# Kernel optimization log

Hardware: AMD Instinct MI355X
Metric: run time of the kernel (lower is better)

Reference implementation:

```python
import jax, jax.numpy as jnp
import numpy as np

STRIDES = (8, 16, 32)
BINS = 16
NC = 80
ALPHA, GAMMA = 0.25, 2.0
W_CLS, W_IOU, W_DFL = 1.0, 7.5, 1.5
B, MAX_GT = 32, 32
EPS = 1e-7


def setup_inputs() -> dict:
    key = jax.random.key(0)
    k0, k1, k2, k3, k4, k5, k6 = jax.random.split(key, 7)
    p0 = jax.random.normal(k0, (B, 4 * BINS + NC, 80, 80), dtype=jnp.float32)
    p1 = jax.random.normal(k1, (B, 4 * BINS + NC, 40, 40), dtype=jnp.float32)
    p2 = jax.random.normal(k2, (B, 4 * BINS + NC, 20, 20), dtype=jnp.float32)
    # realistic xyxy boxes inside a 640x640 image
    c = jax.random.uniform(k3, (B, MAX_GT, 2), minval=60.0, maxval=580.0)
    wh = jax.random.uniform(k4, (B, MAX_GT, 2), minval=16.0, maxval=120.0)
    gt_bboxes = jnp.concatenate([c - wh / 2, c + wh / 2], axis=-1).astype(jnp.float32)
    gt_labels = jax.random.randint(k5, (B, MAX_GT), 0, NC, dtype=jnp.int32)
    raw = jax.random.randint(k6, (B, 8400), 0, 20 * MAX_GT, dtype=jnp.int32)
    matched_gt_inds = jnp.where(raw < MAX_GT, raw, -1)
    return {"p0": p0, "p1": p1, "p2": p2, "gt_bboxes": gt_bboxes,
            "gt_labels": gt_labels, "matched_gt_inds": matched_gt_inds}


def _decode_scale(p, stride):
    # p: [B, 4*BINS + NC, H, W]
    Bp, C, H, W = p.shape
    dfl = p[:, :4 * BINS].reshape(Bp, 4, BINS, H, W)
    cls = p[:, 4 * BINS:]
    # DFL decode: expectation of softmax over bins, scaled by stride
    prob = jax.nn.softmax(dfl, axis=2)
    proj = jnp.arange(BINS, dtype=p.dtype)
    dist = jnp.einsum('bkchw,c->bkhw', prob, proj) * stride  # [B,4,H,W] in pixels
    ys, xs = jnp.meshgrid(jnp.arange(H), jnp.arange(W), indexing='ij')
    cx = ((xs.astype(p.dtype)) + 0.5) * stride
    cy = ((ys.astype(p.dtype)) + 0.5) * stride
    boxes = jnp.stack([cx - dist[:, 0], cy - dist[:, 1],
                       cx + dist[:, 2], cy + dist[:, 3]], axis=-1).reshape(Bp, H * W, 4)
    cls_logits = cls.transpose(0, 2, 3, 1).reshape(Bp, H * W, NC)
    dfl_flat = dfl.transpose(0, 3, 4, 1, 2).reshape(Bp, H * W, 4, BINS)
    grid = jnp.stack([cx, cy], axis=-1).reshape(H * W, 2)
    smap = jnp.full((H * W,), stride, dtype=p.dtype)
    return cls_logits, dfl_flat, boxes, grid, smap


def reference(p0, p1, p2, gt_bboxes, gt_labels, matched_gt_inds):
    outs = [_decode_scale(p, s) for p, s in zip((p0, p1, p2), STRIDES)]
    scores = jnp.concatenate([o[0] for o in outs], axis=1)   # [B,N,NC]
    dfl = jnp.concatenate([o[1] for o in outs], axis=1)      # [B,N,4,BINS]
    pboxes = jnp.concatenate([o[2] for o in outs], axis=1)   # [B,N,4]
    grid = jnp.concatenate([o[3] for o in outs], axis=0)     # [N,2]
    smap = jnp.concatenate([o[4] for o in outs], axis=0)     # [N]

    pos = matched_gt_inds >= 0                               # [B,N]
    idx = jnp.where(pos, matched_gt_inds, 0)
    lbl = jnp.take_along_axis(gt_labels, idx, axis=1)        # [B,N]
    posf = pos.astype(scores.dtype)
    tgt_scores = jax.nn.one_hot(lbl, NC, dtype=scores.dtype) * posf[..., None]

    # sigmoid focal loss (stable BCE-with-logits)
    prob = jax.nn.sigmoid(scores)
    ce = jnp.maximum(scores, 0) - scores * tgt_scores + jnp.log1p(jnp.exp(-jnp.abs(scores)))
    p_t = prob * tgt_scores + (1 - prob) * (1 - tgt_scores)
    alpha_t = tgt_scores * ALPHA + (1 - tgt_scores) * (1 - ALPHA)
    cls_elem = alpha_t * (1.0 - p_t) ** GAMMA * ce
    num_pos = jnp.maximum(posf.sum(), 1.0)
    loss_cls = cls_elem.sum() / num_pos

    # gather matched GT boxes per anchor
    tboxes = jnp.take_along_axis(gt_bboxes, idx[..., None], axis=1)  # [B,N,4]
    gx, gy = grid[None, :, 0], grid[None, :, 1]
    l = jnp.clip(gx - tboxes[..., 0], 0.0)
    t = jnp.clip(gy - tboxes[..., 1], 0.0)
    r = jnp.clip(tboxes[..., 2] - gx, 0.0)
    b_ = jnp.clip(tboxes[..., 3] - gy, 0.0)
    dists = jnp.stack([l, t, r, b_], axis=-1) / smap[None, :, None]   # [B,N,4]
    tb = jnp.clip(dists, 0.0, BINS - 1 - 1e-6)
    lo = jnp.floor(tb).astype(jnp.int32)
    hi = jnp.minimum(lo + 1, BINS - 1)
    a = tb - lo.astype(tb.dtype)
    # soft two-bin DFL target (vectorized form of the scatter_add loop)
    tdist = (jax.nn.one_hot(lo, BINS, dtype=dfl.dtype) * (1.0 - a)[..., None]
             + jax.nn.one_hot(hi, BINS, dtype=dfl.dtype) * a[..., None])   # [B,N,4,BINS]
    logp = jax.nn.log_softmax(dfl, axis=-1)
    dfl_elem = -(tdist * logp).sum(-1)                                # [B,N,4]
    loss_dfl = (dfl_elem * posf[..., None]).sum() / (num_pos * 4.0)

    # IoU loss on positives
    ix1 = jnp.maximum(pboxes[..., 0], tboxes[..., 0])
    iy1 = jnp.maximum(pboxes[..., 1], tboxes[..., 1])
    ix2 = jnp.minimum(pboxes[..., 2], tboxes[..., 2])
    iy2 = jnp.minimum(pboxes[..., 3], tboxes[..., 3])
    inter = jnp.clip(ix2 - ix1, 0.0) * jnp.clip(iy2 - iy1, 0.0)
    area_p = jnp.clip(pboxes[..., 2] - pboxes[..., 0], 0.0) * jnp.clip(pboxes[..., 3] - pboxes[..., 1], 0.0)
    area_t = jnp.clip(tboxes[..., 2] - tboxes[..., 0], 0.0) * jnp.clip(tboxes[..., 3] - tboxes[..., 1], 0.0)
    iou = inter / (area_p + area_t - inter + EPS)
    loss_iou = ((1.0 - iou) * posf).sum() / num_pos

    total = W_CLS * loss_cls + W_IOU * loss_iou + W_DFL * loss_dfl
    return total
```

## Files before the change

### kernel.cpp

```cpp
#include <hip/hip_runtime.h>
#include <math.h>

#define NCLS 80
#define BINS 16
#define BATCH 32
#define MAX_GT 32
#define NA 8400
#define AN (BATCH * NA)
#define NT 2100
#define NB_DFL 1050
#define NB_CLS 2560
#define NSLOT 64
#define ALPHA_C 0.25f
#define W_CLS 1.0
#define W_IOU 7.5
#define W_DFL 1.5
#define EPS_F 1e-7f


__device__ __forceinline__ void block_reduce_atomic(float val, double* __restrict__ target)
{
    __shared__ float s[4];
    __syncthreads();
    #pragma unroll
    for (int o = 32; o > 0; o >>= 1) val += __shfl_down(val, o);
    const int wave = threadIdx.x >> 6, lane = threadIdx.x & 63;
    if (lane == 0) s[wave] = val;
    __syncthreads();
    if (threadIdx.x == 0) atomicAdd(target, (double)(s[0] + s[1] + s[2] + s[3]));
}

__device__ __forceinline__ float focal_elem(float s, float tt)
{
    float e   = __expf(-fabsf(s));
    float inv = 1.f / (1.f + e);
    float prob = (s >= 0.f) ? inv : e * inv;
    float ce  = fmaxf(s, 0.f) - s * tt + __logf(1.f + e);
    float p_t = prob * tt + (1.f - prob) * (1.f - tt);
    float alpha_t = tt * ALPHA_C + (1.f - tt) * (1.f - ALPHA_C);
    float om = 1.f - p_t;
    return alpha_t * om * om * ce;
}

__global__ __launch_bounds__(256) void yolo_prep(
    const int* __restrict__ matched, const int* __restrict__ gt_labels,
    signed char* __restrict__ lblmap, double* __restrict__ acc)
{
    if (blockIdx.x == 0) acc[threadIdx.x] = 0.0;
    const int qid = blockIdx.x * 256 + threadIdx.x;
    if (qid >= AN / 4) return;
    const int a0 = qid * 4;
    const int b  = a0 / NA;
    const int4 m4 = *(const int4*)(matched + a0);
    const int mm[4] = {m4.x, m4.y, m4.z, m4.w};
    char4 o;
    o.x = (mm[0] >= 0) ? (signed char)gt_labels[b * MAX_GT + mm[0]] : (signed char)-1;
    o.y = (mm[1] >= 0) ? (signed char)gt_labels[b * MAX_GT + mm[1]] : (signed char)-1;
    o.z = (mm[2] >= 0) ? (signed char)gt_labels[b * MAX_GT + mm[2]] : (signed char)-1;
    o.w = (mm[3] >= 0) ? (signed char)gt_labels[b * MAX_GT + mm[3]] : (signed char)-1;
    *(char4*)(lblmap + a0) = o;
}

__global__ __launch_bounds__(256) void yolo_mega(
    const float* __restrict__ p0, const float* __restrict__ p1, const float* __restrict__ p2,
    const float* __restrict__ gt_bboxes, const int* __restrict__ matched,
    const signed char* __restrict__ lblmap, double* __restrict__ acc)
{
    const int bid  = blockIdx.x;
    const int slot = bid & (NSLOT - 1);

    if (bid < NB_DFL) {
        __shared__ float spd[64][4][4];
        const int gdt = bid * 256 + (int)threadIdx.x;
        const int k   = gdt & 3;
        const int qg  = gdt >> 2;
        const int b   = qg / NT;
        const int t   = qg - b * NT;

        const float* p; int HW, off, gbase, h, w0; float stride;
        if (t < 1600)      { p = p0; HW = 6400; off = t * 4;          gbase = 0;    stride = 8.f;
                             h = t / 20;  w0 = (t - h * 20) * 4; }
        else if (t < 2000) { p = p1; HW = 1600; off = (t - 1600) * 4; gbase = 6400; stride = 16.f;
                             int u = t - 1600; h = u / 10; w0 = (u - h * 10) * 4; }
        else               { p = p2; HW = 400;  off = (t - 2000) * 4; gbase = 8000; stride = 32.f;
                             int u = t - 2000; h = u / 5;  w0 = (u - h * 5) * 4; }
        const float inv_s = 1.f / stride;
        const float cy = ((float)h + 0.5f) * stride;

        const float* pc = p + (size_t)(b * 144 + k * BINS) * HW + off;
        float v[BINS][4];
        #pragma unroll
        for (int i = 0; i < BINS; ++i) {
            float4 q = *(const float4*)(pc + (size_t)i * HW);
            v[i][0] = q.x; v[i][1] = q.y; v[i][2] = q.z; v[i][3] = q.w;
        }
        const int4 m4 = *(const int4*)(matched + (size_t)b * NA + gbase + off);
        const int mm[4] = {m4.x, m4.y, m4.z, m4.w};
        bool pos[4]; float4 tbv[4]; float tdv[4];
        #pragma unroll
        for (int j = 0; j < 4; ++j) {
            pos[j] = (mm[j] >= 0);
            int idx = pos[j] ? mm[j] : 0;
            tbv[j] = *(const float4*)(gt_bboxes + ((size_t)b * MAX_GT + idx) * 4);
            float cx = ((float)(w0 + j) + 0.5f) * stride;
            float d = (k == 0) ? (cx - tbv[j].x) : (k == 1) ? (cy - tbv[j].y)
                    : (k == 2) ? (tbv[j].z - cx) : (tbv[j].w - cy);
            tdv[j] = fmaxf(d, 0.f) * inv_s;
        }

        float part = 0.f;
        float pd[4];
        #pragma unroll
        for (int j = 0; j < 4; ++j) {
            float tval = fminf(tdv[j], (float)(BINS - 1) - 1e-6f);
            int   lo = (int)floorf(tval);
            float fr = tval - (float)lo;
            float mx = v[0][j];
            #pragma unroll
            for (int i = 1; i < BINS; ++i) mx = fmaxf(mx, v[i][j]);
            float se = 0.f, we = 0.f, vlo = 0.f, vhi = 0.f;
            #pragma unroll
            for (int i = 0; i < BINS; ++i) {
                float e = __expf(v[i][j] - mx);
                se += e;
                we += (float)i * e;
                vlo = (i == lo)     ? v[i][j] : vlo;
                vhi = (i == lo + 1) ? v[i][j] : vhi;
            }
            pd[j] = (we / se) * stride;
            if (pos[j]) {
                float lse = mx + __logf(se);
                part += -((1.f - fr) * (vlo - lse) + fr * (vhi - lse));
            }
        }
        *(float4*)&spd[threadIdx.x >> 2][k][0] = make_float4(pd[0], pd[1], pd[2], pd[3]);
        __syncthreads();

        float iou_part = 0.f, cnt = 0.f;
        if (k == 0) {
            const int g = threadIdx.x >> 2;
            #pragma unroll
            for (int j = 0; j < 4; ++j) {
                if (pos[j]) {
                    float cx = ((float)(w0 + j) + 0.5f) * stride;
                    float px1 = cx - spd[g][0][j], py1 = cy - spd[g][1][j];
                    float px2 = cx + spd[g][2][j], py2 = cy + spd[g][3][j];
                    float4 tb = tbv[j];
                    float ix1 = fmaxf(px1, tb.x), iy1 = fmaxf(py1, tb.y);
                    float ix2 = fminf(px2, tb.z), iy2 = fminf(py2, tb.w);
                    float inter  = fmaxf(ix2 - ix1, 0.f) * fmaxf(iy2 - iy1, 0.f);
                    float area_p = fmaxf(px2 - px1, 0.f) * fmaxf(py2 - py1, 0.f);
                    float area_t = fmaxf(tb.z - tb.x, 0.f) * fmaxf(tb.w - tb.y, 0.f);
                    float iou = inter / (area_p + area_t - inter + EPS_F);
                    iou_part += 1.f - iou;
                    cnt += 1.f;
                }
            }
        }
        block_reduce_atomic(part,     &acc[2 * NSLOT + slot]);
        block_reduce_atomic(iou_part, &acc[1 * NSLOT + slot]);
        block_reduce_atomic(cnt,      &acc[3 * NSLOT + slot]);
    } else {
        const int cbid = bid - NB_DFL;
        const int b = cbid / NCLS;
        const int c = cbid - b * NCLS;
        const size_t cls_ch = (size_t)(b * 144 + 4 * BINS + c);
        const signed char* lb0 = lblmap + b * NA;

        float4 q[9];
        char4  l4[9];
        const float* pl0 = p0 + cls_ch * 6400;
        #pragma unroll
        for (int i = 0; i < 6; ++i) {
            int off = (i * 256 + (int)threadIdx.x) * 4;
            q[i]  = *(const float4*)(pl0 + off);
            l4[i] = *(const char4*)(lb0 + off);
        }
        #pragma unroll
        for (int i = 6; i < 9; ++i) {
            int t  = i * 256 + (int)threadIdx.x;
            int tc = (t < NT) ? t : 0;
            const float* p; int HW, off, gbase;
            if (tc < 1600)      { p = p0; HW = 6400; off = tc * 4;          gbase = 0;    }
            else if (tc < 2000) { p = p1; HW = 1600; off = (tc - 1600) * 4; gbase = 6400; }
            else                { p = p2; HW = 400;  off = (tc - 2000) * 4; gbase = 8000; }
            q[i]  = *(const float4*)(p + cls_ch * HW + off);
            l4[i] = *(const char4*)(lb0 + gbase + off);
        }

        float part = 0.f;
        #pragma unroll
        for (int i = 0; i < 9; ++i) {
            const bool valid = (i < 8) || (i * 256 + (int)threadIdx.x < NT);
            const float s4[4]  = {q[i].x, q[i].y, q[i].z, q[i].w};
            const int   lbl[4] = {l4[i].x, l4[i].y, l4[i].z, l4[i].w};
            float sum = 0.f;
            #pragma unroll
            for (int j = 0; j < 4; ++j)
                sum += focal_elem(s4[j], (c == lbl[j]) ? 1.f : 0.f);
            part += valid ? sum : 0.f;
        }
        block_reduce_atomic(part, &acc[0 * NSLOT + slot]);
    }
}

__global__ __launch_bounds__(256) void yolo_loss_fused(
    const float* __restrict__ p0, const float* __restrict__ p1, const float* __restrict__ p2,
    const float* __restrict__ gt_bboxes, const int* __restrict__ gt_labels,
    const int* __restrict__ matched, double* __restrict__ acc)
{
    const int a = blockIdx.x * blockDim.x + threadIdx.x;
    const int b = blockIdx.y;
    const int slot = blockIdx.x & (NSLOT - 1);
    float cls_acc = 0.f, iou_acc = 0.f, dfl_acc = 0.f, pos_cnt = 0.f;
    if (a < NA) {
        const float* p; int HW, W; float stride; int off;
        if (a < 6400)      { p = p0; HW = 6400; W = 80; stride = 8.f;  off = a; }
        else if (a < 8000) { p = p1; HW = 1600; W = 40; stride = 16.f; off = a - 6400; }
        else               { p = p2; HW = 400;  W = 20; stride = 32.f; off = a - 8000; }
        const int h = off / W, w = off - h * W;
        const float cx = ((float)w + 0.5f) * stride, cy = ((float)h + 0.5f) * stride;
        const float* pb = p + ((size_t)b * 144) * (size_t)HW + (size_t)off;
        const int m = matched[(size_t)b * NA + a];
        const bool pos = (m >= 0);
        const int idx = pos ? m : 0;
        const int lbl = gt_labels[b * MAX_GT + idx];
        const float* tbp = gt_bboxes + ((size_t)b * MAX_GT + idx) * 4;
        const float tx1 = tbp[0], ty1 = tbp[1], tx2 = tbp[2], ty2 = tbp[3];
        float tdist[4] = {fmaxf(cx - tx1, 0.f) / stride, fmaxf(cy - ty1, 0.f) / stride,
                          fmaxf(tx2 - cx, 0.f) / stride, fmaxf(ty2 - cy, 0.f) / stride};
        float pdv[4]; float dfl_sum = 0.f;
        #pragma unroll
        for (int k = 0; k < 4; ++k) {
            float tv = fminf(tdist[k], (float)(BINS - 1) - 1e-6f);
            int lo = (int)floorf(tv);
            float fr = tv - (float)lo;
            const float* pc = pb + (size_t)(k * BINS) * HW;
            float v[BINS];
            #pragma unroll
            for (int i = 0; i < BINS; ++i) v[i] = pc[(size_t)i * HW];
            float mx = v[0];
            #pragma unroll
            for (int i = 1; i < BINS; ++i) mx = fmaxf(mx, v[i]);
            float se = 0.f, we = 0.f, vlo = 0.f, vhi = 0.f;
            #pragma unroll
            for (int i = 0; i < BINS; ++i) {
                float e = __expf(v[i] - mx);
                se += e; we += (float)i * e;
                vlo = (i == lo) ? v[i] : vlo;
                vhi = (i == lo + 1) ? v[i] : vhi;
            }
            pdv[k] = (we / se) * stride;
            if (pos) { float lse = mx + __logf(se); dfl_sum += -((1.f - fr) * (vlo - lse) + fr * (vhi - lse)); }
        }
        const float* pcls = pb + (size_t)(4 * BINS) * HW;
        #pragma unroll 4
        for (int c = 0; c < NCLS; ++c)
            cls_acc += focal_elem(pcls[(size_t)c * HW], (pos && c == lbl) ? 1.f : 0.f);
        if (pos) {
            float px1 = cx - pdv[0], py1 = cy - pdv[1], px2 = cx + pdv[2], py2 = cy + pdv[3];
            float ix1 = fmaxf(px1, tx1), iy1 = fmaxf(py1, ty1);
            float ix2 = fminf(px2, tx2), iy2 = fminf(py2, ty2);
            float inter  = fmaxf(ix2 - ix1, 0.f) * fmaxf(iy2 - iy1, 0.f);
            float area_p = fmaxf(px2 - px1, 0.f) * fmaxf(py2 - py1, 0.f);
            float area_t = fmaxf(tx2 - tx1, 0.f) * fmaxf(ty2 - ty1, 0.f);
            float iou = inter / (area_p + area_t - inter + EPS_F);
            iou_acc = 1.f - iou; dfl_acc = dfl_sum; pos_cnt = 1.f;
        }
    }
    block_reduce_atomic(cls_acc, &acc[0 * NSLOT + slot]);
    block_reduce_atomic(iou_acc, &acc[1 * NSLOT + slot]);
    block_reduce_atomic(dfl_acc, &acc[2 * NSLOT + slot]);
    block_reduce_atomic(pos_cnt, &acc[3 * NSLOT + slot]);
}

__global__ void yolo_loss_finalize(const double* __restrict__ acc, float* __restrict__ out)
{
    double s[4] = {0.0, 0.0, 0.0, 0.0};
    for (int q = 0; q < 4; ++q)
        for (int i = 0; i < NSLOT; ++i) s[q] += acc[q * NSLOT + i];
    double np = s[3] < 1.0 ? 1.0 : s[3];
    double total = W_CLS * s[0] / np + W_IOU * s[1] / np + W_DFL * s[2] / (np * 4.0);
    out[0] = (float)total;
}

extern "C" void kernel_launch(void* const* d_in, const int* in_sizes, int n_in,
                              void* d_out, int out_size, void* d_ws, size_t ws_size,
                              hipStream_t stream)
{
    const float* p0        = (const float*)d_in[0];
    const float* p1        = (const float*)d_in[1];
    const float* p2        = (const float*)d_in[2];
    const float* gt_bboxes = (const float*)d_in[3];
    const int*   gt_labels = (const int*)d_in[4];
    const int*   matched   = (const int*)d_in[5];
    float*  out = (float*)d_out;

    const size_t accBytes = 4 * NSLOT * sizeof(double);
    double*      acc    = (double*)d_ws;
    signed char* lblmap = (signed char*)((char*)d_ws + accBytes);
    const size_t need = accBytes + (size_t)AN;

    if (ws_size >= need) {
        yolo_prep<<<(AN / 4 + 255) / 256, 256, 0, stream>>>(matched, gt_labels, lblmap, acc);
        yolo_mega<<<NB_DFL + NB_CLS, 256, 0, stream>>>(p0, p1, p2, gt_bboxes, matched,
                                                       lblmap, acc);
    } else {
        (void)hipMemsetAsync(acc, 0, accBytes, stream);
        dim3 g((NA + 255) / 256, BATCH);
        yolo_loss_fused<<<g, 256, 0, stream>>>(p0, p1, p2, gt_bboxes, gt_labels, matched, acc);
    }
    yolo_loss_finalize<<<1, 1, 0, stream>>>(acc, out);
}
```

Before: 215.6 us.

## Drop label-map prep via focal correction, online softmax, per-block partials

Removes the label-map prep kernel. The class branch now computes the focal loss assuming every target is zero, and the DFL branch adds a per-positive correction term (focal(t=1) - focal(t=0)) at the matched label's logit. The DFL softmax becomes a streaming online max/sum over groups of four bins, and the two target-bin logits are reloaded instead of kept in registers. Shared-memory exchange of distances is replaced by wave shuffles, and the atomic slot accumulation is replaced by per-block partial writes reduced in a parallel finalize kernel. The intent is to cut a launch, byte-map traffic, register pressure and atomics, in exchange for a few extra scattered loads.

```diff
diff --git a/kernel.cpp b/kernel.cpp
--- a/kernel.cpp
+++ b/kernel.cpp
@@ -10,25 +10,13 @@
 #define NT 2100
 #define NB_DFL 1050
 #define NB_CLS 2560
+#define NBLK (NB_DFL + NB_CLS)
 #define NSLOT 64
 #define ALPHA_C 0.25f
 #define W_CLS 1.0
 #define W_IOU 7.5
 #define W_DFL 1.5
 #define EPS_F 1e-7f
-
-
-__device__ __forceinline__ void block_reduce_atomic(float val, double* __restrict__ target)
-{
-    __shared__ float s[4];
-    __syncthreads();
-    #pragma unroll
-    for (int o = 32; o > 0; o >>= 1) val += __shfl_down(val, o);
-    const int wave = threadIdx.x >> 6, lane = threadIdx.x & 63;
-    if (lane == 0) s[wave] = val;
-    __syncthreads();
-    if (threadIdx.x == 0) atomicAdd(target, (double)(s[0] + s[1] + s[2] + s[3]));
-}
 
 __device__ __forceinline__ float focal_elem(float s, float tt)
 {
@@ -42,35 +30,37 @@
     return alpha_t * om * om * ce;
 }
 
-__global__ __launch_bounds__(256) void yolo_prep(
-    const int* __restrict__ matched, const int* __restrict__ gt_labels,
-    signed char* __restrict__ lblmap, double* __restrict__ acc)
-{
-    if (blockIdx.x == 0) acc[threadIdx.x] = 0.0;
-    const int qid = blockIdx.x * 256 + threadIdx.x;
-    if (qid >= AN / 4) return;
-    const int a0 = qid * 4;
-    const int b  = a0 / NA;
-    const int4 m4 = *(const int4*)(matched + a0);
-    const int mm[4] = {m4.x, m4.y, m4.z, m4.w};
-    char4 o;
-    o.x = (mm[0] >= 0) ? (signed char)gt_labels[b * MAX_GT + mm[0]] : (signed char)-1;
-    o.y = (mm[1] >= 0) ? (signed char)gt_labels[b * MAX_GT + mm[1]] : (signed char)-1;
-    o.z = (mm[2] >= 0) ? (signed char)gt_labels[b * MAX_GT + mm[2]] : (signed char)-1;
-    o.w = (mm[3] >= 0) ? (signed char)gt_labels[b * MAX_GT + mm[3]] : (signed char)-1;
-    *(char4*)(lblmap + a0) = o;
+__device__ __forceinline__ void block_write4(float c0, float c1, float c2, float c3,
+                                             double* __restrict__ blk)
+{
+    #pragma unroll
+    for (int o = 32; o > 0; o >>= 1) {
+        c0 += __shfl_down(c0, o);
+        c1 += __shfl_down(c1, o);
+        c2 += __shfl_down(c2, o);
+        c3 += __shfl_down(c3, o);
+    }
+    __shared__ float s4[4][4];
+    const int wave = threadIdx.x >> 6, lane = threadIdx.x & 63;
+    if (lane == 0) { s4[wave][0] = c0; s4[wave][1] = c1; s4[wave][2] = c2; s4[wave][3] = c3; }
+    __syncthreads();
+    if (threadIdx.x == 0) {
+        double* o = blk + (size_t)blockIdx.x * 4;
+        o[0] = (double)(s4[0][0] + s4[1][0] + s4[2][0] + s4[3][0]);
+        o[1] = (double)(s4[0][1] + s4[1][1] + s4[2][1] + s4[3][1]);
+        o[2] = (double)(s4[0][2] + s4[1][2] + s4[2][2] + s4[3][2]);
+        o[3] = (double)(s4[0][3] + s4[1][3] + s4[2][3] + s4[3][3]);
+    }
 }
 
 __global__ __launch_bounds__(256) void yolo_mega(
     const float* __restrict__ p0, const float* __restrict__ p1, const float* __restrict__ p2,
-    const float* __restrict__ gt_bboxes, const int* __restrict__ matched,
-    const signed char* __restrict__ lblmap, double* __restrict__ acc)
-{
-    const int bid  = blockIdx.x;
-    const int slot = bid & (NSLOT - 1);
+    const float* __restrict__ gt_bboxes, const int* __restrict__ gt_labels,
+    const int* __restrict__ matched, double* __restrict__ blk)
+{
+    const int bid = blockIdx.x;
 
     if (bid < NB_DFL) {
-        __shared__ float spd[64][4][4];
         const int gdt = bid * 256 + (int)threadIdx.x;
         const int k   = gdt & 3;
         const int qg  = gdt >> 2;
@@ -86,66 +76,83 @@
                              int u = t - 2000; h = u / 5;  w0 = (u - h * 5) * 4; }
         const float inv_s = 1.f / stride;
         const float cy = ((float)h + 0.5f) * stride;
-
         const float* pc = p + (size_t)(b * 144 + k * BINS) * HW + off;
-        float v[BINS][4];
-        #pragma unroll
-        for (int i = 0; i < BINS; ++i) {
-            float4 q = *(const float4*)(pc + (size_t)i * HW);
-            v[i][0] = q.x; v[i][1] = q.y; v[i][2] = q.z; v[i][3] = q.w;
-        }
+
         const int4 m4 = *(const int4*)(matched + (size_t)b * NA + gbase + off);
         const int mm[4] = {m4.x, m4.y, m4.z, m4.w};
-        bool pos[4]; float4 tbv[4]; float tdv[4];
+        int lo[4]; float fr[4];
         #pragma unroll
         for (int j = 0; j < 4; ++j) {
-            pos[j] = (mm[j] >= 0);
-            int idx = pos[j] ? mm[j] : 0;
-            tbv[j] = *(const float4*)(gt_bboxes + ((size_t)b * MAX_GT + idx) * 4);
-            float cx = ((float)(w0 + j) + 0.5f) * stride;
-            float d = (k == 0) ? (cx - tbv[j].x) : (k == 1) ? (cy - tbv[j].y)
-                    : (k == 2) ? (tbv[j].z - cx) : (tbv[j].w - cy);
-            tdv[j] = fmaxf(d, 0.f) * inv_s;
+            const int idx = (mm[j] >= 0) ? mm[j] : 0;
+            const float4 tb = *(const float4*)(gt_bboxes + ((size_t)b * MAX_GT + idx) * 4);
+            const float cx = ((float)(w0 + j) + 0.5f) * stride;
+            float d = (k == 0) ? (cx - tb.x) : (k == 1) ? (cy - tb.y)
+                    : (k == 2) ? (tb.z - cx) : (tb.w - cy);
+            float tval = fminf(fmaxf(d, 0.f) * inv_s, (float)(BINS - 1) - 1e-6f);
+            lo[j] = (int)tval;
+            fr[j] = tval - (float)lo[j];
+        }
+
+        float mr[4], se[4], we[4];
+        #pragma unroll
+        for (int j = 0; j < 4; ++j) { mr[j] = -1e30f; se[j] = 0.f; we[j] = 0.f; }
+        #pragma unroll
+        for (int i0 = 0; i0 < BINS; i0 += 4) {
+            float4 qa = *(const float4*)(pc + (size_t)(i0 + 0) * HW);
+            float4 qb = *(const float4*)(pc + (size_t)(i0 + 1) * HW);
+            float4 qc = *(const float4*)(pc + (size_t)(i0 + 2) * HW);
+            float4 qd = *(const float4*)(pc + (size_t)(i0 + 3) * HW);
+            const float r0[4] = {qa.x, qa.y, qa.z, qa.w};
+            const float r1[4] = {qb.x, qb.y, qb.z, qb.w};
+            const float r2[4] = {qc.x, qc.y, qc.z, qc.w};
+            const float r3[4] = {qd.x, qd.y, qd.z, qd.w};
+            #pragma unroll
+            for (int j = 0; j < 4; ++j) {
+                float v0 = r0[j], v1 = r1[j], v2 = r2[j], v3 = r3[j];
+                float mx = fmaxf(fmaxf(v0, v1), fmaxf(v2, v3));
+                float mn = fmaxf(mr[j], mx);
+                float sc = __expf(mr[j] - mn);
+                float e0 = __expf(v0 - mn), e1 = __expf(v1 - mn);
+                float e2 = __expf(v2 - mn), e3 = __expf(v3 - mn);
+                se[j] = se[j] * sc + ((e0 + e1) + (e2 + e3));
+                we[j] = we[j] * sc + ((float)(i0    ) * e0 + (float)(i0 + 1) * e1
+                                    + (float)(i0 + 2) * e2 + (float)(i0 + 3) * e3);
+                mr[j] = mn;
+            }
         }
 
         float part = 0.f;
         float pd[4];
         #pragma unroll
         for (int j = 0; j < 4; ++j) {
-            float tval = fminf(tdv[j], (float)(BINS - 1) - 1e-6f);
-            int   lo = (int)floorf(tval);
-            float fr = tval - (float)lo;
-            float mx = v[0][j];
-            #pragma unroll
-            for (int i = 1; i < BINS; ++i) mx = fmaxf(mx, v[i][j]);
-            float se = 0.f, we = 0.f, vlo = 0.f, vhi = 0.f;
-            #pragma unroll
-            for (int i = 0; i < BINS; ++i) {
-                float e = __expf(v[i][j] - mx);
-                se += e;
-                we += (float)i * e;
-                vlo = (i == lo)     ? v[i][j] : vlo;
-                vhi = (i == lo + 1) ? v[i][j] : vhi;
+            pd[j] = (we[j] / se[j]) * stride;
+            if (mm[j] >= 0) {
+                float vlo = pc[(size_t)lo[j] * HW + j];
+                float vhi = pc[(size_t)(lo[j] + 1) * HW + j];
+                float lse = mr[j] + __logf(se[j]);
+                part += -((1.f - fr[j]) * (vlo - lse) + fr[j] * (vhi - lse));
             }
-            pd[j] = (we / se) * stride;
-            if (pos[j]) {
-                float lse = mx + __logf(se);
-                part += -((1.f - fr) * (vlo - lse) + fr * (vhi - lse));
-            }
-        }
-        *(float4*)&spd[threadIdx.x >> 2][k][0] = make_float4(pd[0], pd[1], pd[2], pd[3]);
-        __syncthreads();
-
-        float iou_part = 0.f, cnt = 0.f;
+        }
+
+        const int lbase = ((int)threadIdx.x & 63) & ~3;
+        float d0[4], d1[4], d2[4], d3[4];
+        #pragma unroll
+        for (int j = 0; j < 4; ++j) {
+            d0[j] = __shfl(pd[j], lbase + 0);
+            d1[j] = __shfl(pd[j], lbase + 1);
+            d2[j] = __shfl(pd[j], lbase + 2);
+            d3[j] = __shfl(pd[j], lbase + 3);
+        }
+
+        float iou_part = 0.f, cnt = 0.f, cls_corr = 0.f;
         if (k == 0) {
-            const int g = threadIdx.x >> 2;
             #pragma unroll
             for (int j = 0; j < 4; ++j) {
-                if (pos[j]) {
-                    float cx = ((float)(w0 + j) + 0.5f) * stride;
-                    float px1 = cx - spd[g][0][j], py1 = cy - spd[g][1][j];
-                    float px2 = cx + spd[g][2][j], py2 = cy + spd[g][3][j];
-                    float4 tb = tbv[j];
+                if (mm[j] >= 0) {
+                    const float cx = ((float)(w0 + j) + 0.5f) * stride;
+                    float px1 = cx - d0[j], py1 = cy - d1[j];
+                    float px2 = cx + d2[j], py2 = cy + d3[j];
+                    const float4 tb = *(const float4*)(gt_bboxes + ((size_t)b * MAX_GT + mm[j]) * 4);
                     float ix1 = fmaxf(px1, tb.x), iy1 = fmaxf(py1, tb.y);
                     float ix2 = fminf(px2, tb.z), iy2 = fminf(py2, tb.w);
                     float inter  = fmaxf(ix2 - ix1, 0.f) * fmaxf(iy2 - iy1, 0.f);
@@ -154,54 +161,84 @@
                     float iou = inter / (area_p + area_t - inter + EPS_F);
                     iou_part += 1.f - iou;
                     cnt += 1.f;
+                    int lbl = gt_labels[b * MAX_GT + mm[j]];
+                    float sv = *(p + (size_t)(b * 144 + 4 * BINS + lbl) * HW + off + j);
+                    cls_corr += focal_elem(sv, 1.f) - focal_elem(sv, 0.f);
                 }
             }
         }
-        block_reduce_atomic(part,     &acc[2 * NSLOT + slot]);
-        block_reduce_atomic(iou_part, &acc[1 * NSLOT + slot]);
-        block_reduce_atomic(cnt,      &acc[3 * NSLOT + slot]);
+        block_write4(cls_corr, iou_part, part, cnt, blk);
     } else {
         const int cbid = bid - NB_DFL;
         const int b = cbid / NCLS;
         const int c = cbid - b * NCLS;
         const size_t cls_ch = (size_t)(b * 144 + 4 * BINS + c);
-        const signed char* lb0 = lblmap + b * NA;
 
         float4 q[9];
-        char4  l4[9];
         const float* pl0 = p0 + cls_ch * 6400;
         #pragma unroll
         for (int i = 0; i < 6; ++i) {
             int off = (i * 256 + (int)threadIdx.x) * 4;
-            q[i]  = *(const float4*)(pl0 + off);
-            l4[i] = *(const char4*)(lb0 + off);
+            q[i] = *(const float4*)(pl0 + off);
         }
         #pragma unroll
         for (int i = 6; i < 9; ++i) {
             int t  = i * 256 + (int)threadIdx.x;
             int tc = (t < NT) ? t : 0;
-            const float* p; int HW, off, gbase;
-            if (tc < 1600)      { p = p0; HW = 6400; off = tc * 4;          gbase = 0;    }
-            else if (tc < 2000) { p = p1; HW = 1600; off = (tc - 1600) * 4; gbase = 6400; }
-            else                { p = p2; HW = 400;  off = (tc - 2000) * 4; gbase = 8000; }
-            q[i]  = *(const float4*)(p + cls_ch * HW + off);
-            l4[i] = *(const char4*)(lb0 + gbase + off);
+            const float* p; int HW, off;
+            if (tc < 1600)      { p = p0; HW = 6400; off = tc * 4; }
+            else if (tc < 2000) { p = p1; HW = 1600; off = (tc - 1600) * 4; }
+            else                { p = p2; HW = 400;  off = (tc - 2000) * 4; }
+            q[i] = *(const float4*)(p + cls_ch * HW + off);
         }
 
         float part = 0.f;
         #pragma unroll
         for (int i = 0; i < 9; ++i) {
             const bool valid = (i < 8) || (i * 256 + (int)threadIdx.x < NT);
-            const float s4[4]  = {q[i].x, q[i].y, q[i].z, q[i].w};
-            const int   lbl[4] = {l4[i].x, l4[i].y, l4[i].z, l4[i].w};
-            float sum = 0.f;
-            #pragma unroll
-            for (int j = 0; j < 4; ++j)
-                sum += focal_elem(s4[j], (c == lbl[j]) ? 1.f : 0.f);
+            float sum = focal_elem(q[i].x, 0.f) + focal_elem(q[i].y, 0.f)
+                      + focal_elem(q[i].z, 0.f) + focal_elem(q[i].w, 0.f);
             part += valid ? sum : 0.f;
         }
-        block_reduce_atomic(part, &acc[0 * NSLOT + slot]);
-    }
+        block_write4(part, 0.f, 0.f, 0.f, blk);
+    }
+}
+
+__global__ __launch_bounds__(256) void yolo_finalize_blocks(
+    const double* __restrict__ blk, float* __restrict__ out)
+{
+    double s0 = 0.0, s1 = 0.0, s2 = 0.0, s3 = 0.0;
+    for (int r = (int)threadIdx.x; r < NBLK; r += 256) {
+        const double* row = blk + (size_t)r * 4;
+        s0 += row[0]; s1 += row[1]; s2 += row[2]; s3 += row[3];
+    }
+    #pragma unroll
+    for (int o = 32; o > 0; o >>= 1) {
+        s0 += __shfl_down(s0, o); s1 += __shfl_down(s1, o);
+        s2 += __shfl_down(s2, o); s3 += __shfl_down(s3, o);
+    }
+    __shared__ double sh[4][4];
+    const int wave = threadIdx.x >> 6, lane = threadIdx.x & 63;
+    if (lane == 0) { sh[wave][0] = s0; sh[wave][1] = s1; sh[wave][2] = s2; sh[wave][3] = s3; }
+    __syncthreads();
+    if (threadIdx.x == 0) {
+        double c = 0, i = 0, d = 0, n = 0;
+        for (int w = 0; w < 4; ++w) { c += sh[w][0]; i += sh[w][1]; d += sh[w][2]; n += sh[w][3]; }
+        double np = (n < 1.0) ? 1.0 : n;
+        out[0] = (float)(W_CLS * c / np + W_IOU * i / np + W_DFL * d / (np * 4.0));
+    }
+}
+
+__device__ __forceinline__ void block_reduce_atomic(float val, double* __restrict__ target)
+{
+    __shared__ float s[4];
+    __syncthreads();
+    #pragma unroll
+    for (int o = 32; o > 0; o >>= 1) val += __shfl_down(val, o);
+    const int wave = threadIdx.x >> 6, lane = threadIdx.x & 63;
+    if (lane == 0) s[wave] = val;
+    __syncthreads();
+    if (threadIdx.x == 0) atomicAdd(target, (double)(s[0] + s[1] + s[2] + s[3]));
 }
 
 __global__ __launch_bounds__(256) void yolo_loss_fused(
@@ -235,10 +272,10 @@
             float tv = fminf(tdist[k], (float)(BINS - 1) - 1e-6f);
             int lo = (int)floorf(tv);
             float fr = tv - (float)lo;
-            const float* pc = pb + (size_t)(k * BINS) * HW;
+            const float* pcx = pb + (size_t)(k * BINS) * HW;
             float v[BINS];
             #pragma unroll
-            for (int i = 0; i < BINS; ++i) v[i] = pc[(size_t)i * HW];
+            for (int i = 0; i < BINS; ++i) v[i] = pcx[(size_t)i * HW];
             float mx = v[0];
             #pragma unroll
             for (int i = 1; i < BINS; ++i) mx = fmaxf(mx, v[i]);
@@ -296,19 +333,17 @@
     const int*   matched   = (const int*)d_in[5];
     float*  out = (float*)d_out;
 
-    const size_t accBytes = 4 * NSLOT * sizeof(double);
-    double*      acc    = (double*)d_ws;
-    signed char* lblmap = (signed char*)((char*)d_ws + accBytes);
-    const size_t need = accBytes + (size_t)AN;
+    const size_t need = (size_t)NBLK * 4 * sizeof(double);
 
     if (ws_size >= need) {
-        yolo_prep<<<(AN / 4 + 255) / 256, 256, 0, stream>>>(matched, gt_labels, lblmap, acc);
-        yolo_mega<<<NB_DFL + NB_CLS, 256, 0, stream>>>(p0, p1, p2, gt_bboxes, matched,
-                                                       lblmap, acc);
+        double* blk = (double*)d_ws;
+        yolo_mega<<<NBLK, 256, 0, stream>>>(p0, p1, p2, gt_bboxes, gt_labels, matched, blk);
+        yolo_finalize_blocks<<<1, 256, 0, stream>>>(blk, out);
     } else {
-        (void)hipMemsetAsync(acc, 0, accBytes, stream);
+        double* acc = (double*)d_ws;
+        (void)hipMemsetAsync(acc, 0, 4 * NSLOT * sizeof(double), stream);
         dim3 g((NA + 255) / 256, BATCH);
         yolo_loss_fused<<<g, 256, 0, stream>>>(p0, p1, p2, gt_bboxes, gt_labels, matched, acc);
-    }
-    yolo_loss_finalize<<<1, 1, 0, stream>>>(acc, out);
-}
+        yolo_loss_finalize<<<1, 1, 0, stream>>>(acc, out);
+    }
+}
```

Measured after the change: 217.8 us. No clear change (+1.0%).
